# Optimization experiments

Measured on AMD Instinct MI355X. Metric: run time of the kernel, lower is better.

The kernel has to match this reference:

```python
import jax, jax.numpy as jnp
import numpy as np

B, S, HOPS, DIM, NREL = 1024, 32, 2, 64, 237
NENT, NEDGE = 14541, 272115
SIGMA = 0.1
CFMW = 64


def setup_inputs() -> dict:
    key = jax.random.key(0)
    ks = jax.random.split(key, 20)

    def g(k, shape):
        return (jax.random.normal(k, shape, dtype=jnp.float32) / np.float32(np.sqrt(shape[0])))

    inp = {
        "entity_pairs": jax.random.randint(ks[0], (B, 2), 0, NENT),
        "train_edges": jax.random.randint(ks[1], (B,), 0, NEDGE),
        "labels": jax.random.randint(ks[2], (B,), 0, NREL),
        "entity2edges": jax.random.randint(ks[3], (NENT + 1, S), 0, NEDGE + 1),
        "edge2entities": jax.random.randint(ks[4], (NEDGE + 1, 1), 0, NENT + 1),
        "edge2relation": jax.random.randint(ks[5], (NEDGE + 1,), 0, NREL + 1),
        "t": jax.random.uniform(ks[6], (B,), dtype=jnp.float32),
        "eps": jax.random.normal(ks[7], (B, NREL), dtype=jnp.float32),
        "rel_feat": g(ks[8], (NREL, DIM)),
        "W_agg0": g(ks[9], (DIM, DIM)), "b_agg0": jnp.zeros((DIM,), jnp.float32),
        "W_agg1": g(ks[10], (DIM, NREL)), "b_agg1": jnp.zeros((NREL,), jnp.float32),
        "W_out": g(ks[11], (2 * NREL, NREL)), "b_out": jnp.zeros((NREL,), jnp.float32),
        "mW1": g(ks[12], (NREL + 1, CFMW)), "mb1": jnp.zeros((CFMW,), jnp.float32),
        "mW2": g(ks[13], (CFMW, CFMW)), "mb2": jnp.zeros((CFMW,), jnp.float32),
        "mW3": g(ks[14], (CFMW, CFMW)), "mb3": jnp.zeros((CFMW,), jnp.float32),
        "mW4": g(ks[15], (CFMW, NREL)), "mb4": jnp.zeros((NREL,), jnp.float32),
    }
    return inp


def _side(ent, labels, train_edges, entity2edges, edge2entities, edge2relation, relf, aggs):
    # multi-hop neighbor edge gather + masks (exclude the training edge itself)
    edges_list = [labels]  # hop-0 "edges" are the relation labels
    masks = []
    for i in range(HOPS):
        if i == 0:
            ne = ent.reshape(B, 1)  # (B, 1) source entities
        else:
            ne = edge2entities[edges_list[-1].reshape(-1)].reshape(B, -1)
        nedges = entity2edges[ne.reshape(-1)].reshape(B, -1)  # (B, S**(i+1))
        edges_list.append(nedges)
        masks.append((nedges != train_edges[:, None]).astype(relf.dtype))
    # edge -> relation -> feature
    ev = [relf[edges_list[0]]]  # (B, DIM)
    for edges in edges_list[1:]:
        ev.append(relf[edge2relation[edges]])  # (B, S**h, DIM)
    # iterative mean aggregation (PathCon-style, one entity per edge)
    for i in range(HOPS):
        W, b, act, self_inc = aggs[i]
        d = W.shape[0]
        nxt = []
        for hop in range(HOPS - i):
            neigh = ev[hop + 1].reshape(B, -1, 1, S, d)
            m = masks[hop].reshape(B, -1, 1, S, 1)
            out = jnp.mean(jnp.mean(neigh * m, axis=-2), axis=-2)  # (B, S**hop, d)
            if self_inc:
                out = out + ev[hop].reshape(B, -1, d)
            nxt.append(act(out @ W + b))
        ev = nxt
    return ev[0].reshape(B, NREL)


def reference(entity_pairs, train_edges, labels, entity2edges, edge2entities,
              edge2relation, t, eps, rel_feat, W_agg0, b_agg0, W_agg1, b_agg1,
              W_out, b_out, mW1, mb1, mW2, mb2, mW3, mb3, mW4, mb4):
    relf = jnp.concatenate([rel_feat, jnp.zeros((1, DIM), rel_feat.dtype)], axis=0)
    aggs = [
        (W_agg0, b_agg0, jax.nn.relu, True),    # intermediate hop: relu, self-included
        (W_agg1, b_agg1, lambda x: x, False),   # last hop: identity, no self
    ]
    x0 = _side(entity_pairs[:, 0], labels, train_edges, entity2edges,
               edge2entities, edge2relation, relf, aggs)
    x1 = _side(entity_pairs[:, 1], labels, train_edges, entity2edges,
               edge2entities, edge2relation, relf, aggs)
    output = jnp.concatenate([x0, x1], axis=-1) @ W_out + b_out  # (B, NREL)
    # CFM: xt = (1-t) x0 + t x1 + sigma*eps ; ut = x1 - x0
    tb = t[:, None]
    xt = (1.0 - tb) * x0 + tb * x1 + SIGMA * eps
    h = jnp.concatenate([xt, tb], axis=-1)
    h = jax.nn.selu(h @ mW1 + mb1)
    h = jax.nn.selu(h @ mW2 + mb2)
    h = jax.nn.selu(h @ mW3 + mb3)
    vt = h @ mW4 + mb4
    scores = output * vt
    return scores
```

## Files before the change

kernel.cpp:

```cpp
#include <hip/hip_runtime.h>
#include <math.h>

#define BB 1024
#define S 32
#define DIM 64
#define NREL 237
#define NENT 14541
#define SIGMA 0.1f

#define OFS_WR    0
#define N_WR      (238*64)
#define OFS_WC0   15232
#define N_WC      (64*237)
#define OFS_WC1   (OFS_WC0 + N_WC)
#define OFS_BC    (OFS_WC1 + N_WC)
#define OFS_HC    (OFS_BC + 237)
#define OFS_A     45872

#define LDS_BYTES 18688

__device__ __forceinline__ float selu_f(float x) {
    const float alpha = 1.6732632423543772f;
    const float scale = 1.0507009873554805f;
    return scale * (x > 0.f ? x : alpha * expm1f(x));
}

__global__ __launch_bounds__(256) void precompute_kernel(
    const float* __restrict__ rel_feat, const float* __restrict__ W0,
    const float* __restrict__ W1, const float* __restrict__ b1,
    const float* __restrict__ W_out, const float* __restrict__ b_out,
    const float* __restrict__ mW1, const float* __restrict__ mb1,
    float* __restrict__ ws) {
    __shared__ float red[256];
    int blk = blockIdx.x;
    const int tid = threadIdx.x;

    if (blk < 60) {
        int idx = blk * 256 + tid;
        if (idx < 238 * 64) {
            int r = idx >> 6, o = idx & 63;
            float acc = 0.f;
            if (r < NREL) {
#pragma unroll 8
                for (int d = 0; d < 64; ++d)
                    acc += rel_feat[r * 64 + d] * W0[d * 64 + o];
            }
            ws[OFS_WR + idx] = acc;
        }
        return;
    }
    blk -= 60;
    if (blk < 512) {
        int half = blk >> 8;
        int lb = blk & 255;
        int o = lb >> 2, ct = lb & 3;
        int cl = tid & 63, g = tid >> 6;
        int c = ct * 64 + cl;
        const float* Wsrc = W_out + half * 237 * 237;
        float acc = 0.f;
        if (c < NREL) {
            int k0 = g * 60, k1 = (g == 3) ? 237 : (k0 + 60);
#pragma unroll 4
            for (int k = k0; k < k1; ++k)
                acc += W1[o * 237 + k] * Wsrc[k * 237 + c];
        }
        red[tid] = acc;
        __syncthreads();
        if (g == 0 && c < NREL) {
            float s = red[cl] + red[64 + cl] + red[128 + cl] + red[192 + cl];
            ws[(half ? OFS_WC1 : OFS_WC0) + o * 237 + c] = s;
        }
        return;
    }
    blk -= 512;
    if (blk < 4) {
        int cl = tid & 63, g = tid >> 6;
        int c = blk * 64 + cl;
        float acc = 0.f;
        if (c < NREL) {
            int k0 = g * 60, k1 = (g == 3) ? 237 : (k0 + 60);
#pragma unroll 4
            for (int k = k0; k < k1; ++k)
                acc += b1[k] * (W_out[k * 237 + c] + W_out[(237 + k) * 237 + c]);
        }
        red[tid] = acc;
        __syncthreads();
        if (g == 0 && c < NREL)
            ws[OFS_BC + c] = b_out[c] + red[cl] + red[64 + cl] + red[128 + cl] + red[192 + cl];
        return;
    }
    {
        int w = tid & 63, g = tid >> 6;
        int k0 = g * 60, k1 = (g == 3) ? 237 : (k0 + 60);
        float acc = 0.f;
#pragma unroll 4
        for (int k = k0; k < k1; ++k)
            acc += b1[k] * mW1[k * 64 + w];
        red[tid] = acc;
        __syncthreads();
        if (g == 0)
            ws[OFS_HC + w] = mb1[w] + red[w] + red[64 + w] + red[128 + w] + red[192 + w];
    }
}

__global__ __launch_bounds__(256) void agg_kernel(
    const int* __restrict__ e2e_tab, const int* __restrict__ e2r,
    float* __restrict__ ws) {
    __shared__ int s_r[512];
    const int tid = threadIdx.x;
    const int grp = tid >> 4, c = tid & 15;
    const int ent = blockIdx.x * 16 + grp;
    const bool ok = ent < (NENT + 1);
    if (ok) {
        int ea = e2e_tab[ent * S + c];
        int eb = e2e_tab[ent * S + 16 + c];
        s_r[grp * 32 + c] = e2r[ea];
        s_r[grp * 32 + 16 + c] = e2r[eb];
    }
    __syncthreads();
    if (ok) {
        const float4* Wr4 = (const float4*)(ws + OFS_WR);
        const int* rr = &s_r[grp * 32];
        float4 acc = make_float4(0.f, 0.f, 0.f, 0.f);
#pragma unroll
        for (int s = 0; s < 32; ++s) {
            float4 v = Wr4[rr[s] * 16 + c];
            acc.x += v.x; acc.y += v.y; acc.z += v.z; acc.w += v.w;
        }
        ((float4*)(ws + OFS_A))[ent * 16 + c] = acc;
    }
}

__global__ __launch_bounds__(512, 8) void gf_kernel(
    const int* __restrict__ ep, const int* __restrict__ te_arr,
    const int* __restrict__ e2e_tab, const int* __restrict__ e2ent,
    const int* __restrict__ e2r, const float* __restrict__ b0,
    const float* __restrict__ t_arr, const float* __restrict__ eps,
    const float* __restrict__ W1, const float* __restrict__ mW1,
    const float* __restrict__ mW2, const float* __restrict__ mb2,
    const float* __restrict__ mW3, const float* __restrict__ mb3,
    const float* __restrict__ mW4, const float* __restrict__ mb4,
    const float* __restrict__ ws, float* __restrict__ out) {
    extern __shared__ float smem[];
    float* s_v1   = smem;
    int*   s_r1   = (int*)(smem + 4352);
    int*   s_ent2 = (int*)(smem + 4416);
    float* s_m1   = smem + 4480;
    float* s_ov   = smem + 4544;

    const int tid = threadIdx.x;
    const int b = blockIdx.x;
    const int grp = tid >> 4;
    const int c = tid & 15;
    const int te = te_arr[b];
    const int rte = e2r[te];
    const float4* Wr4 = (const float4*)(ws + OFS_WR);
    const float4* A4  = (const float4*)(ws + OFS_A);
    const float4 b0v  = ((const float4*)b0)[c];
    const float4 wrte = Wr4[rte * 16 + c];

    if (tid < 64) {
        int u = tid >> 5, s = tid & 31;
        int ent = ep[b * 2 + u];
        int e1 = e2e_tab[ent * S + s];
        s_r1[u * 32 + s] = e2r[e1];
        s_m1[u * 32 + s] = (e1 != te) ? 1.0f : 0.0f;
        s_ent2[u * 32 + s] = e2ent[e1];
    }
    __syncthreads();

    const float inv = 1.0f / 32.0f;
#pragma unroll
    for (int u = 0; u < 2; ++u) {
        const int j = grp;
        const int ent2 = s_ent2[u * 32 + j];
        int e2a = e2e_tab[ent2 * S + c];
        int e2b = e2e_tab[ent2 * S + 16 + c];
        int cnt = (e2a == te) + (e2b == te);
        cnt += __shfl_xor(cnt, 1);
        cnt += __shfl_xor(cnt, 2);
        cnt += __shfl_xor(cnt, 4);
        cnt += __shfl_xor(cnt, 8);
        float4 a4   = A4[ent2 * 16 + c];
        float4 self = Wr4[s_r1[u * 32 + j] * 16 + c];
        float fc = (float)cnt;
        float m = s_m1[u * 32 + j];
        float4 r;
        r.x = fmaxf(self.x + (a4.x - fc * wrte.x) * inv + b0v.x, 0.f) * m;
        r.y = fmaxf(self.y + (a4.y - fc * wrte.y) * inv + b0v.y, 0.f) * m;
        r.z = fmaxf(self.z + (a4.z - fc * wrte.z) * inv + b0v.z, 0.f) * m;
        r.w = fmaxf(self.w + (a4.w - fc * wrte.w) * inv + b0v.w, 0.f) * m;
        *((float4*)&s_v1[(u * 32 + j) * 68 + c * 4]) = r;
    }
    __syncthreads();
    if (tid < 128) {
        int u = tid >> 6, w = tid & 63;
        float sum = 0.f;
#pragma unroll 8
        for (int j = 0; j < 32; ++j) sum += s_v1[(u * 32 + j) * 68 + w];
        s_ov[u * 64 + w] = sum * inv;
    }
    __syncthreads();

    float* s_ymix = smem;
    float* s_outv = smem + 240;
    float* s_red  = smem + 480;
    float* s_h    = smem + 992;
    float* s_omix = smem + 1056;
    float* s_vp   = smem + 1120;
    const float tb = t_arr[b];
    const float* Wc0 = ws + OFS_WC0;
    const float* Wc1 = ws + OFS_WC1;
    const float* bc = ws + OFS_BC;
    const float* hc = ws + OFS_HC;

    if (tid < 64)
        s_omix[tid] = (1.f - tb) * s_ov[tid] + tb * s_ov[64 + tid];
    __syncthreads();

    if (tid < 256) {
        if (tid < NREL) {
            float y = 0.f;
#pragma unroll 4
            for (int d = 0; d < 64; ++d)
                y += s_omix[d] * W1[d * 237 + tid];
            s_ymix[tid] = y;
        }
    } else {
        int cc = tid - 256;
        if (cc < NREL) {
            float a = bc[cc];
#pragma unroll 4
            for (int d = 0; d < 64; ++d)
                a += s_ov[d] * Wc0[d * 237 + cc] + s_ov[64 + d] * Wc1[d * 237 + cc];
            s_outv[cc] = a;
        }
    }
    __syncthreads();

    {
        int w = tid & 63, q = tid >> 6;
        int k0 = q * 30, k1 = (q == 7) ? 237 : (k0 + 30);
        const float* e = eps + b * 237;
        float a = 0.f;
#pragma unroll 4
        for (int k = k0; k < k1; ++k)
            a += (SIGMA * e[k] + s_ymix[k]) * mW1[k * 64 + w];
        s_red[tid] = a;
    }
    __syncthreads();
    if (tid < 64) {
        float h = hc[tid] + tb * mW1[237 * 64 + tid];
#pragma unroll
        for (int q = 0; q < 8; ++q) h += s_red[q * 64 + tid];
        s_h[tid] = selu_f(h);
    }
    __syncthreads();

    {
        int w = tid & 63, q = tid >> 6;
        float a = 0.f;
#pragma unroll
        for (int d = q * 8; d < q * 8 + 8; ++d)
            a += s_h[d] * mW2[d * 64 + w];
        s_red[tid] = a;
    }
    __syncthreads();
    if (tid < 64) {
        float v = mb2[tid];
#pragma unroll
        for (int q = 0; q < 8; ++q) v += s_red[q * 64 + tid];
        s_h[tid] = selu_f(v);
    }
    __syncthreads();

    {
        int w = tid & 63, q = tid >> 6;
        float a = 0.f;
#pragma unroll
        for (int d = q * 8; d < q * 8 + 8; ++d)
            a += s_h[d] * mW3[d * 64 + w];
        s_red[tid] = a;
    }
    __syncthreads();
    if (tid < 64) {
        float v = mb3[tid];
#pragma unroll
        for (int q = 0; q < 8; ++q) v += s_red[q * 64 + tid];
        s_h[tid] = selu_f(v);
    }
    __syncthreads();

    {
        int half = tid >> 8, cc = tid & 255;
        if (cc < NREL) {
            float a = 0.f;
#pragma unroll 4
            for (int w = half * 32; w < half * 32 + 32; ++w)
                a += s_h[w] * mW4[w * 237 + cc];
            s_vp[half * 240 + cc] = a;
        }
    }
    __syncthreads();
    if (tid < NREL)
        out[b * 237 + tid] = s_outv[tid] * (mb4[tid] + s_vp[tid] + s_vp[240 + tid]);
}

extern "C" void kernel_launch(void* const* d_in, const int* in_sizes, int n_in,
                              void* d_out, int out_size, void* d_ws, size_t ws_size,
                              hipStream_t stream) {
    const int* ep       = (const int*)d_in[0];
    const int* te       = (const int*)d_in[1];
    const int* e2e      = (const int*)d_in[3];
    const int* e2ent    = (const int*)d_in[4];
    const int* e2r      = (const int*)d_in[5];
    const float* t      = (const float*)d_in[6];
    const float* eps    = (const float*)d_in[7];
    const float* relf   = (const float*)d_in[8];
    const float* W0     = (const float*)d_in[9];
    const float* b0     = (const float*)d_in[10];
    const float* W1     = (const float*)d_in[11];
    const float* b1     = (const float*)d_in[12];
    const float* W_out  = (const float*)d_in[13];
    const float* b_out  = (const float*)d_in[14];
    const float* mW1    = (const float*)d_in[15];
    const float* mb1    = (const float*)d_in[16];
    const float* mW2    = (const float*)d_in[17];
    const float* mb2    = (const float*)d_in[18];
    const float* mW3    = (const float*)d_in[19];
    const float* mb3    = (const float*)d_in[20];
    const float* mW4    = (const float*)d_in[21];
    const float* mb4    = (const float*)d_in[22];
    float* ws  = (float*)d_ws;
    float* out = (float*)d_out;

    hipLaunchKernelGGL(precompute_kernel, dim3(577), dim3(256), 0, stream,
                       relf, W0, W1, b1, W_out, b_out, mW1, mb1, ws);
    hipLaunchKernelGGL(agg_kernel, dim3((NENT + 1 + 15) / 16), dim3(256), 0, stream,
                       e2e, e2r, ws);
    hipLaunchKernelGGL(gf_kernel, dim3(BB), dim3(512), LDS_BYTES, stream,
                       ep, te, e2e, e2ent, e2r, b0,
                       t, eps, W1, mW1, mW2, mb2, mW3, mb3, mW4, mb4, ws, out);
}
```

Before: 142.1 us.

## Split Wr precompute and merge entity aggregation with weight folding kernel

The Wr = rel_feat@W0 product moves into its own small kernel. The entity-neighbour aggregation, which depends only on Wr, is merged with the independent W1·W_out, bias and mW1 folding work into one 512-thread kernel. This lets the folding run alongside the aggregation instead of serialising with it, and the folding reductions now split K across 8 groups instead of 4. It also regroups the kernel boundaries: the aggregation now waits on a tiny kernel instead of the larger precompute, and all the folding blocks share a launch with the aggregation blocks.

```diff
diff --git a/kernel.cpp b/kernel.cpp
--- a/kernel.cpp
+++ b/kernel.cpp
@@ -25,109 +25,118 @@
     return scale * (x > 0.f ? x : alpha * expm1f(x));
 }
 
-__global__ __launch_bounds__(256) void precompute_kernel(
+__global__ __launch_bounds__(256) void pre_wr_kernel(
     const float* __restrict__ rel_feat, const float* __restrict__ W0,
+    float* __restrict__ ws) {
+    int idx = blockIdx.x * 256 + threadIdx.x;
+    if (idx < 238 * 64) {
+        int r = idx >> 6, o = idx & 63;
+        float acc = 0.f;
+        if (r < NREL) {
+#pragma unroll 8
+            for (int d = 0; d < 64; ++d)
+                acc += rel_feat[r * 64 + d] * W0[d * 64 + o];
+        }
+        ws[OFS_WR + idx] = acc;
+    }
+}
+
+__global__ __launch_bounds__(512) void mid_kernel(
+    const int* __restrict__ e2e_tab, const int* __restrict__ e2r,
     const float* __restrict__ W1, const float* __restrict__ b1,
     const float* __restrict__ W_out, const float* __restrict__ b_out,
     const float* __restrict__ mW1, const float* __restrict__ mb1,
     float* __restrict__ ws) {
-    __shared__ float red[256];
+    __shared__ int   s_r[1024];
+    __shared__ float red[512];
     int blk = blockIdx.x;
     const int tid = threadIdx.x;
 
-    if (blk < 60) {
-        int idx = blk * 256 + tid;
-        if (idx < 238 * 64) {
-            int r = idx >> 6, o = idx & 63;
-            float acc = 0.f;
-            if (r < NREL) {
-#pragma unroll 8
-                for (int d = 0; d < 64; ++d)
-                    acc += rel_feat[r * 64 + d] * W0[d * 64 + o];
+    if (blk < 455) {
+        const int grp = tid >> 4, c = tid & 15;
+        const int ent = blk * 32 + grp;
+        const bool ok = ent < (NENT + 1);
+        if (ok) {
+            int ea = e2e_tab[ent * S + c];
+            int eb = e2e_tab[ent * S + 16 + c];
+            s_r[grp * 32 + c] = e2r[ea];
+            s_r[grp * 32 + 16 + c] = e2r[eb];
+        }
+        __syncthreads();
+        if (ok) {
+            const float4* Wr4 = (const float4*)(ws + OFS_WR);
+            const int* rr = &s_r[grp * 32];
+            float4 acc = make_float4(0.f, 0.f, 0.f, 0.f);
+#pragma unroll
+            for (int s = 0; s < 32; ++s) {
+                float4 v = Wr4[rr[s] * 16 + c];
+                acc.x += v.x; acc.y += v.y; acc.z += v.z; acc.w += v.w;
             }
-            ws[OFS_WR + idx] = acc;
+            ((float4*)(ws + OFS_A))[ent * 16 + c] = acc;
         }
         return;
     }
-    blk -= 60;
+    blk -= 455;
     if (blk < 512) {
         int half = blk >> 8;
         int lb = blk & 255;
         int o = lb >> 2, ct = lb & 3;
-        int cl = tid & 63, g = tid >> 6;
+        int cl = tid & 63, q = tid >> 6;
         int c = ct * 64 + cl;
         const float* Wsrc = W_out + half * 237 * 237;
         float acc = 0.f;
         if (c < NREL) {
-            int k0 = g * 60, k1 = (g == 3) ? 237 : (k0 + 60);
+            int k0 = q * 30, k1 = (q == 7) ? 237 : (k0 + 30);
 #pragma unroll 4
             for (int k = k0; k < k1; ++k)
                 acc += W1[o * 237 + k] * Wsrc[k * 237 + c];
         }
         red[tid] = acc;
         __syncthreads();
-        if (g == 0 && c < NREL) {
-            float s = red[cl] + red[64 + cl] + red[128 + cl] + red[192 + cl];
+        if (q == 0 && c < NREL) {
+            float s = 0.f;
+#pragma unroll
+            for (int qq = 0; qq < 8; ++qq) s += red[qq * 64 + cl];
             ws[(half ? OFS_WC1 : OFS_WC0) + o * 237 + c] = s;
         }
         return;
     }
     blk -= 512;
     if (blk < 4) {
-        int cl = tid & 63, g = tid >> 6;
+        int cl = tid & 63, q = tid >> 6;
         int c = blk * 64 + cl;
         float acc = 0.f;
         if (c < NREL) {
-            int k0 = g * 60, k1 = (g == 3) ? 237 : (k0 + 60);
+            int k0 = q * 30, k1 = (q == 7) ? 237 : (k0 + 30);
 #pragma unroll 4
             for (int k = k0; k < k1; ++k)
                 acc += b1[k] * (W_out[k * 237 + c] + W_out[(237 + k) * 237 + c]);
         }
         red[tid] = acc;
         __syncthreads();
-        if (g == 0 && c < NREL)
-            ws[OFS_BC + c] = b_out[c] + red[cl] + red[64 + cl] + red[128 + cl] + red[192 + cl];
+        if (q == 0 && c < NREL) {
+            float s = b_out[c];
+#pragma unroll
+            for (int qq = 0; qq < 8; ++qq) s += red[qq * 64 + cl];
+            ws[OFS_BC + c] = s;
+        }
         return;
     }
     {
-        int w = tid & 63, g = tid >> 6;
-        int k0 = g * 60, k1 = (g == 3) ? 237 : (k0 + 60);
+        int w = tid & 63, q = tid >> 6;
+        int k0 = q * 30, k1 = (q == 7) ? 237 : (k0 + 30);
         float acc = 0.f;
 #pragma unroll 4
         for (int k = k0; k < k1; ++k)
             acc += b1[k] * mW1[k * 64 + w];
         red[tid] = acc;
         __syncthreads();
-        if (g == 0)
-            ws[OFS_HC + w] = mb1[w] + red[w] + red[64 + w] + red[128 + w] + red[192 + w];
-    }
-}
-
-__global__ __launch_bounds__(256) void agg_kernel(
-    const int* __restrict__ e2e_tab, const int* __restrict__ e2r,
-    float* __restrict__ ws) {
-    __shared__ int s_r[512];
-    const int tid = threadIdx.x;
-    const int grp = tid >> 4, c = tid & 15;
-    const int ent = blockIdx.x * 16 + grp;
-    const bool ok = ent < (NENT + 1);
-    if (ok) {
-        int ea = e2e_tab[ent * S + c];
-        int eb = e2e_tab[ent * S + 16 + c];
-        s_r[grp * 32 + c] = e2r[ea];
-        s_r[grp * 32 + 16 + c] = e2r[eb];
-    }
-    __syncthreads();
-    if (ok) {
-        const float4* Wr4 = (const float4*)(ws + OFS_WR);
-        const int* rr = &s_r[grp * 32];
-        float4 acc = make_float4(0.f, 0.f, 0.f, 0.f);
-#pragma unroll
-        for (int s = 0; s < 32; ++s) {
-            float4 v = Wr4[rr[s] * 16 + c];
-            acc.x += v.x; acc.y += v.y; acc.z += v.z; acc.w += v.w;
-        }
-        ((float4*)(ws + OFS_A))[ent * 16 + c] = acc;
+        if (q == 0) {
+            float s = mb1[w];
+#pragma unroll
+            for (int qq = 0; qq < 8; ++qq) s += red[qq * 64 + w];
+            ws[OFS_HC + w] = s;
+        }
     }
 }
 
@@ -334,10 +343,10 @@
     float* ws  = (float*)d_ws;
     float* out = (float*)d_out;
 
-    hipLaunchKernelGGL(precompute_kernel, dim3(577), dim3(256), 0, stream,
-                       relf, W0, W1, b1, W_out, b_out, mW1, mb1, ws);
-    hipLaunchKernelGGL(agg_kernel, dim3((NENT + 1 + 15) / 16), dim3(256), 0, stream,
-                       e2e, e2r, ws);
+    hipLaunchKernelGGL(pre_wr_kernel, dim3(60), dim3(256), 0, stream,
+                       relf, W0, ws);
+    hipLaunchKernelGGL(mid_kernel, dim3(972), dim3(512), 0, stream,
+                       e2e, e2r, W1, b1, W_out, b_out, mW1, mb1, ws);
     hipLaunchKernelGGL(gf_kernel, dim3(BB), dim3(512), LDS_BYTES, stream,
                        ep, te, e2e, e2ent, e2r, b0,
                        t, eps, W1, mW1, mW2, mb2, mW3, mb3, mW4, mb4, ws, out);
```

Measured after the change: 141.8 us (median of 2 runs). About the same (-0.2%).
